# Performance work log

Measured on AMD Instinct MI355X. Metric: run time of the kernel, lower is better.

## Reference

```python
import jax, jax.numpy as jnp
import numpy as np

EPS = 1e-5

def layer_norm(x, g, b):
    mu = jnp.mean(x, axis=-1, keepdims=True)
    var = jnp.mean(jnp.square(x - mu), axis=-1, keepdims=True)
    return (x - mu) * jax.lax.rsqrt(var + EPS) * g + b

def setup_inputs() -> dict:
    key = jax.random.key(0)
    ks = jax.random.split(key, 8)
    B, T, D, H = 8, 2048, 32, 4
    hd = D // H
    s = 0.05
    return {
        "x": jax.random.normal(ks[0], (B, T, D), jnp.float32),
        "Wq": jax.random.normal(ks[1], (H, D, hd), jnp.float32) * s,
        "Wk": jax.random.normal(ks[2], (H, D, hd), jnp.float32) * s,
        "Wv": jax.random.normal(ks[3], (H, D, hd), jnp.float32) * s,
        "Wproj": jax.random.normal(ks[4], (D, D), jnp.float32) * s,
        "bproj": jnp.zeros((D,), jnp.float32),
        "ln1_g": jnp.ones((D,), jnp.float32),
        "ln1_b": jnp.zeros((D,), jnp.float32),
        "W1": jax.random.normal(ks[5], (D, 4 * D), jnp.float32) * s,
        "b1": jnp.zeros((4 * D,), jnp.float32),
        "W2": jax.random.normal(ks[6], (4 * D, D), jnp.float32) * s,
        "b2": jnp.zeros((D,), jnp.float32),
        "ln2_g": jnp.ones((D,), jnp.float32),
        "ln2_b": jnp.zeros((D,), jnp.float32),
    }

def reference(x, Wq, Wk, Wv, Wproj, bproj, ln1_g, ln1_b, W1, b1, W2, b2, ln2_g, ln2_b):
    B, T, D = x.shape
    H, _, hd = Wq.shape
    scale = hd ** -0.5
    # NOTE: original block normalizes first, and the residual uses the NORMALIZED x
    h = layer_norm(x, ln1_g, ln1_b)                      # (B,T,D)
    q = jnp.einsum('btd,hdk->bhtk', h, Wq)
    k = jnp.einsum('btd,hdk->bhtk', h, Wk)
    v = jnp.einsum('btd,hdk->bhtk', h, Wv)
    scores = jnp.einsum('bhtk,bhsk->bhts', q, k) * scale  # (B,H,T,T)
    mask = jnp.tril(jnp.ones((T, T), bool))
    scores = jnp.where(mask, scores, -jnp.inf)
    attn = jax.nn.softmax(scores, axis=-1)               # dropout = identity (eval)
    o = jnp.einsum('bhts,bhsk->bhtk', attn, v)           # (B,H,T,hd)
    o = o.transpose(0, 2, 1, 3).reshape(B, T, D)         # concat heads, head0 first
    x1 = h + o @ Wproj + bproj
    h2 = layer_norm(x1, ln2_g, ln2_b)
    ff = jax.nn.relu(h2 @ W1 + b1) @ W2 + b2             # dropout = identity (eval)
    return h2 + ff
```

## Files before the change

### kernel.cpp

```cpp
#include <hip/hip_runtime.h>
#include <math.h>

#define BB 8
#define TT 2048
#define DD 32
#define HH 4
#define HD 8
#define NROWS (BB*TT)
#define LNEPS 1e-5f

#if __has_builtin(__builtin_amdgcn_exp2f)
#define EXP2F(x) __builtin_amdgcn_exp2f(x)
#else
#define EXP2F(x) __expf(0.6931471805599453f*(x))
#endif

typedef _Float16 h2 __attribute__((ext_vector_type(2)));
typedef _Float16 h4v __attribute__((ext_vector_type(4)));
typedef _Float16 h8v __attribute__((ext_vector_type(8)));
typedef float f32x16 __attribute__((ext_vector_type(16)));
struct KH { h2 a, b, c, d; };
union F4H { float4 f; KH k; };

static __device__ __forceinline__ h2 pkrtz(float a, float b) {
    return __builtin_bit_cast(h2, __builtin_amdgcn_cvt_pkrtz(a, b));
}
static __device__ __forceinline__ unsigned pkrtz_u(float a, float b) {
    return __builtin_bit_cast(unsigned, __builtin_amdgcn_cvt_pkrtz(a, b));
}
static __device__ __forceinline__ unsigned short f16u(float x) {
    return __builtin_bit_cast(unsigned short, (_Float16)x);
}

#if __has_builtin(__builtin_amdgcn_fdot2)
#define DOT2(a,b,c) __builtin_amdgcn_fdot2((a),(b),(c),false)
#else
#define DOT2(a,b,c) fmaf((float)(a)[1],(float)(b)[1], fmaf((float)(a)[0],(float)(b)[0],(c)))
#endif

__global__ __launch_bounds__(256) void k_ln_qkv(
    const float* __restrict__ x,
    const float* __restrict__ Wq, const float* __restrict__ Wk, const float* __restrict__ Wv,
    const float* __restrict__ g, const float* __restrict__ b,
    float* __restrict__ h, float* __restrict__ qh,
    float* __restrict__ Kh, float* __restrict__ Vt)
{
    __shared__ float sW[3*HH*264];
    __shared__ float sg[DD], sb[DD];
    for (int i = threadIdx.x; i < HH*DD*HD; i += 256) {
        int hd_ = i >> 8, off = i & 255;
        sW[hd_*264 + off]              = Wq[i];
        sW[(4+hd_)*264 + off]          = Wk[i];
        sW[(8+hd_)*264 + off]          = Wv[i];
    }
    if (threadIdx.x < DD) { sg[threadIdx.x] = g[threadIdx.x]; sb[threadIdx.x] = b[threadIdx.x]; }
    __syncthreads();

    int idx = blockIdx.x * 256 + threadIdx.x;
    int r   = idx >> 3;
    int sub = idx & 7;
    int hh  = sub & 3;
    int dh  = sub >> 2;
    int bb  = r >> 11, tt = r & 2047;

    float xr[16];
    {
        const float4* xp = (const float4*)(x + (size_t)r * DD + dh*16);
        float4 t0 = xp[0], t1 = xp[1], t2 = xp[2], t3 = xp[3];
        xr[0]=t0.x; xr[1]=t0.y; xr[2]=t0.z; xr[3]=t0.w;
        xr[4]=t1.x; xr[5]=t1.y; xr[6]=t1.z; xr[7]=t1.w;
        xr[8]=t2.x; xr[9]=t2.y; xr[10]=t2.z; xr[11]=t2.w;
        xr[12]=t3.x; xr[13]=t3.y; xr[14]=t3.z; xr[15]=t3.w;
    }
    float s1 = 0.f;
    #pragma unroll
    for (int i = 0; i < 16; ++i) s1 += xr[i];
    s1 += __shfl_xor(s1, 4, 64);
    float mu = s1 * (1.f/DD);
    float sq = 0.f;
    #pragma unroll
    for (int i = 0; i < 16; ++i) { float d = xr[i]-mu; sq += d*d; }
    sq += __shfl_xor(sq, 4, 64);
    float rs = rsqrtf(sq * (1.f/DD) + LNEPS);

    float hr[16];
    #pragma unroll
    for (int i = 0; i < 16; ++i) hr[i] = (xr[i]-mu)*rs*sg[dh*16+i] + sb[dh*16+i];

    {
        float4* hp = (float4*)(h + (size_t)r * DD + dh*16);
        hp[0]=make_float4(hr[0],hr[1],hr[2],hr[3]);
        hp[1]=make_float4(hr[4],hr[5],hr[6],hr[7]);
        hp[2]=make_float4(hr[8],hr[9],hr[10],hr[11]);
        hp[3]=make_float4(hr[12],hr[13],hr[14],hr[15]);
    }

    const float* wq = sW + hh*264 + dh*128;
    const float* wk = sW + (4+hh)*264 + dh*128;
    const float* wv = sW + (8+hh)*264 + dh*128;
    float qa[HD], ka[HD], va[HD];
    #pragma unroll
    for (int k2 = 0; k2 < HD; ++k2) { qa[k2]=0.f; ka[k2]=0.f; va[k2]=0.f; }
    #pragma unroll
    for (int d = 0; d < 16; ++d) {
        float hv = hr[d];
        const float4* wq4 = (const float4*)(wq + d*8);
        const float4* wk4 = (const float4*)(wk + d*8);
        const float4* wv4 = (const float4*)(wv + d*8);
        float4 a0 = wq4[0], a1 = wq4[1];
        float4 b0 = wk4[0], b1 = wk4[1];
        float4 c0 = wv4[0], c1 = wv4[1];
        qa[0]=fmaf(hv,a0.x,qa[0]); qa[1]=fmaf(hv,a0.y,qa[1]); qa[2]=fmaf(hv,a0.z,qa[2]); qa[3]=fmaf(hv,a0.w,qa[3]);
        qa[4]=fmaf(hv,a1.x,qa[4]); qa[5]=fmaf(hv,a1.y,qa[5]); qa[6]=fmaf(hv,a1.z,qa[6]); qa[7]=fmaf(hv,a1.w,qa[7]);
        ka[0]=fmaf(hv,b0.x,ka[0]); ka[1]=fmaf(hv,b0.y,ka[1]); ka[2]=fmaf(hv,b0.z,ka[2]); ka[3]=fmaf(hv,b0.w,ka[3]);
        ka[4]=fmaf(hv,b1.x,ka[4]); ka[5]=fmaf(hv,b1.y,ka[5]); ka[6]=fmaf(hv,b1.z,ka[6]); ka[7]=fmaf(hv,b1.w,ka[7]);
        va[0]=fmaf(hv,c0.x,va[0]); va[1]=fmaf(hv,c0.y,va[1]); va[2]=fmaf(hv,c0.z,va[2]); va[3]=fmaf(hv,c0.w,va[3]);
        va[4]=fmaf(hv,c1.x,va[4]); va[5]=fmaf(hv,c1.y,va[5]); va[6]=fmaf(hv,c1.z,va[6]); va[7]=fmaf(hv,c1.w,va[7]);
    }
    #pragma unroll
    for (int k2 = 0; k2 < HD; ++k2) {
        qa[k2] += __shfl_xor(qa[k2], 4, 64);
        ka[k2] += __shfl_xor(ka[k2], 4, 64);
        va[k2] += __shfl_xor(va[k2], 4, 64);
    }

    const float SCL = 0.35355339059327373f * 1.4426950408889634f;
    size_t key = (size_t)(bb*HH + hh)*TT + tt;
    unsigned short* vtb = (unsigned short*)Vt + (size_t)(bb*HH + hh)*8*TT + tt;
    if (dh == 0) {
        F4H u;
        u.k.a = pkrtz(qa[0]*SCL, qa[1]*SCL);
        u.k.b = pkrtz(qa[2]*SCL, qa[3]*SCL);
        u.k.c = pkrtz(qa[4]*SCL, qa[5]*SCL);
        u.k.d = pkrtz(qa[6]*SCL, qa[7]*SCL);
        *(float4*)(qh + key*4) = u.f;
        vtb[(size_t)0*TT] = f16u(va[0]);
        vtb[(size_t)1*TT] = f16u(va[1]);
        vtb[(size_t)2*TT] = f16u(va[2]);
        vtb[(size_t)3*TT] = f16u(va[3]);
    } else {
        char* Kb8 = (char*)Kh + (size_t)(bb*HH + hh)*32768;
        uint2 k01; k01.x = pkrtz_u(ka[0],ka[1]); k01.y = pkrtz_u(ka[2],ka[3]);
        uint2 k23; k23.x = pkrtz_u(ka[4],ka[5]); k23.y = pkrtz_u(ka[6],ka[7]);
        *(uint2*)(Kb8 + (size_t)tt*8) = k01;
        *(uint2*)(Kb8 + 16384 + (size_t)tt*8) = k23;
        vtb[(size_t)4*TT] = f16u(va[4]);
        vtb[(size_t)5*TT] = f16u(va[5]);
        vtb[(size_t)6*TT] = f16u(va[6]);
        vtb[(size_t)7*TT] = f16u(va[7]);
    }
}

template<bool DIAG>
__device__ __forceinline__ void chunk_compute(
    uint2 kraw, uint4 v0r, uint4 v1r, int hi, int col,
    h4v qf, float& m, float& l, f32x16& acc)
{
    h4v kf = __builtin_bit_cast(h4v, kraw);
    f32x16 cin;
    #pragma unroll
    for (int r2 = 0; r2 < 16; ++r2) cin[r2] = -m;
    f32x16 S = __builtin_amdgcn_mfma_f32_32x32x8f16(kf, qf, cin, 0, 0, 0);
    if (DIAG) {
        #pragma unroll
        for (int r2 = 0; r2 < 16; ++r2) {
            int row = (r2&3) + 8*(r2>>2) + 4*hi;
            if (row > col) S[r2] = -1e30f;
        }
    }
    float pm = S[0];
    #pragma unroll
    for (int r2 = 1; r2 < 16; ++r2) pm = fmaxf(pm, S[r2]);
    pm = fmaxf(pm, __shfl_xor(pm, 32, 64));
    if (__builtin_expect(__any(pm > 8.f), 0)) {
        float adj = fmaxf(pm, 0.f);
        float cr  = EXP2F(-adj);
        l *= cr;
        #pragma unroll
        for (int r2 = 0; r2 < 16; ++r2) {
            int row = (r2&3) + 8*(r2>>2) + 4*hi;
            acc[r2] *= __shfl(cr, row, 64);
        }
        #pragma unroll
        for (int r2 = 0; r2 < 16; ++r2) S[r2] -= adj;
        m += adj;
    }
    float p[16];
    #pragma unroll
    for (int r2 = 0; r2 < 16; ++r2) p[r2] = EXP2F(S[r2]);
    unsigned pa_ = pkrtz_u(p[0],  p[1]);
    unsigned pb_ = pkrtz_u(p[2],  p[3]);
    unsigned pc_ = pkrtz_u(p[4],  p[5]);
    unsigned pd_ = pkrtz_u(p[6],  p[7]);
    unsigned pe_ = pkrtz_u(p[8],  p[9]);
    unsigned pf_ = pkrtz_u(p[10], p[11]);
    unsigned pg_ = pkrtz_u(p[12], p[13]);
    unsigned ph_ = pkrtz_u(p[14], p[15]);
    const h2 one2 = {(_Float16)1.f, (_Float16)1.f};
    l = DOT2(__builtin_bit_cast(h2, pa_), one2, l);
    l = DOT2(__builtin_bit_cast(h2, pb_), one2, l);
    l = DOT2(__builtin_bit_cast(h2, pc_), one2, l);
    l = DOT2(__builtin_bit_cast(h2, pd_), one2, l);
    l = DOT2(__builtin_bit_cast(h2, pe_), one2, l);
    l = DOT2(__builtin_bit_cast(h2, pf_), one2, l);
    l = DOT2(__builtin_bit_cast(h2, pg_), one2, l);
    l = DOT2(__builtin_bit_cast(h2, ph_), one2, l);
    unsigned ra = (unsigned)__shfl_xor((int)pa_, 32, 64);
    unsigned rb = (unsigned)__shfl_xor((int)pb_, 32, 64);
    unsigned rc = (unsigned)__shfl_xor((int)pc_, 32, 64);
    unsigned rd = (unsigned)__shfl_xor((int)pd_, 32, 64);
    unsigned re = (unsigned)__shfl_xor((int)pe_, 32, 64);
    unsigned rf = (unsigned)__shfl_xor((int)pf_, 32, 64);
    unsigned rg = (unsigned)__shfl_xor((int)pg_, 32, 64);
    unsigned rh = (unsigned)__shfl_xor((int)ph_, 32, 64);
    bool H = (hi != 0);
    uint4 A0 = { H?rc:pa_, H?rd:pb_, H?pc_:ra, H?pd_:rb };
    uint4 A1 = { H?rg:pe_, H?rh:pf_, H?pg_:re, H?ph_:rf };
    acc = __builtin_amdgcn_mfma_f32_32x32x16_f16(
        __builtin_bit_cast(h8v, A0), __builtin_bit_cast(h8v, v0r), acc, 0, 0, 0);
    acc = __builtin_amdgcn_mfma_f32_32x32x16_f16(
        __builtin_bit_cast(h8v, A1), __builtin_bit_cast(h8v, v1r), acc, 0, 0, 0);
}

__global__ __launch_bounds__(256) void k_attn(
    const float* __restrict__ qh, const float* __restrict__ Kh,
    const float* __restrict__ Vt, float* __restrict__ o)
{
    __shared__ float mb[128];
    __shared__ float lb[128];
    __shared__ float ob[512];
    const int tid  = threadIdx.x;
    const int wave = tid >> 6;
    const int lane = tid & 63;
    const int hi   = lane >> 5;
    const int col  = lane & 31;
    const int tl   = wave >> 1;
    const int p    = wave & 1;
    const int T    = blockIdx.x * 2 + tl;
    const int qi   = 63 - (T >> 5);
    const int bh   = T & 31;
    const int wq0  = qi << 5;

    const char* Kg = (const char*)Kh + (size_t)bh * 32768;
    const char* Vg = (const char*)Vt + (size_t)bh * 32768;
    const char* Qg = (const char*)qh + (size_t)bh * 32768 + (size_t)wq0 * 16;
    const char* vrow = Vg + (size_t)(col & 7) * 4096;

    h4v qf = __builtin_bit_cast(h4v, *(const uint2*)(Qg + col*16 + hi*8));

    f32x16 acc;
    #pragma unroll
    for (int r2 = 0; r2 < 16; ++r2) acc[r2] = 0.f;
    float m = 0.f, l = 0.f;

#define LOADC(c, K2, V0, V1) do { \
    K2 = *(const uint2*)(Kg + hi*16384 + (size_t)((((c)<<5) + col))*8); \
    V0 = *(const uint4*)(vrow + (size_t)((((c)<<5) + (hi<<3)))*2); \
    V1 = *(const uint4*)(vrow + (size_t)((((c)<<5) + 16 + (hi<<3)))*2); \
} while (0)

    const int last = ((qi & 1) == p) ? qi : qi - 1;
    if (last >= p) {
        uint2 kc_; uint4 v0c, v1c;
        LOADC(p, kc_, v0c, v1c);
        int c = p;
        while (c < last) {
            uint2 kn_; uint4 v0n, v1n;
            LOADC(c + 2, kn_, v0n, v1n);
            chunk_compute<false>(kc_, v0c, v1c, hi, col, qf, m, l, acc);
            kc_ = kn_; v0c = v0n; v1c = v1n;
            c += 2;
        }
        if (last == qi) chunk_compute<true >(kc_, v0c, v1c, hi, col, qf, m, l, acc);
        else            chunk_compute<false>(kc_, v0c, v1c, hi, col, qf, m, l, acc);
    }
#undef LOADC

    l += __shfl_xor(l, 32, 64);
    if (lane < 32) {
        mb[tl*64 + p*32 + col] = m;
        lb[tl*64 + p*32 + col] = l;
    }
    __syncthreads();
    float mo = mb[tl*64 + (p^1)*32 + col];
    float lo = lb[tl*64 + (p^1)*32 + col];
    float M  = fmaxf(m, mo);
    float fs = EXP2F(m - M);
    float L  = l * fs + lo * EXP2F(mo - M);
    float Linv = 1.f / L;
    float fr[16], Lr[16];
    #pragma unroll
    for (int r2 = 0; r2 < 16; ++r2) {
        int row = (r2&3) + 8*(r2>>2) + 4*hi;
        fr[r2] = __shfl(fs,   row, 64);
        Lr[r2] = __shfl(Linv, row, 64);
    }
    if (p == 1 && col < HD) {
        #pragma unroll
        for (int r2 = 0; r2 < 16; ++r2) {
            int row = (r2&3) + 8*(r2>>2) + 4*hi;
            ob[tl*256 + (row<<3) + col] = acc[r2] * fr[r2];
        }
    }
    __syncthreads();
    if (p == 0 && col < HD) {
        float* og = o + ((size_t)bh*TT + wq0)*HD + col;
        #pragma unroll
        for (int r2 = 0; r2 < 16; ++r2) {
            int row = (r2&3) + 8*(r2>>2) + 4*hi;
            og[(size_t)row * HD] = (acc[r2]*fr[r2] + ob[tl*256 + (row<<3) + col]) * Lr[r2];
        }
    }
}

__global__ __launch_bounds__(256) void k_proj_ffn(
    const float* __restrict__ h, const float* __restrict__ o,
    const float* __restrict__ Wproj, const float* __restrict__ bproj,
    const float* __restrict__ W1, const float* __restrict__ b1,
    const float* __restrict__ W2, const float* __restrict__ b2,
    const float* __restrict__ g2, const float* __restrict__ bt2,
    float* __restrict__ out)
{
    __shared__ float sWp[DD*36], sW1T[4*DD*36], sW2[4*DD*36];
    __shared__ float sbp[DD], sb1[4*DD], sb2[DD], sg2[DD], sbt2[DD];
    for (int i = threadIdx.x; i < DD*DD; i += 256)      sWp [(i>>5)*36 + (i&31)] = Wproj[i];
    for (int i = threadIdx.x; i < DD*4*DD; i += 256) {
        sW1T[(i&127)*36 + (i>>7)] = W1[i];
        sW2 [(i>>5)*36 + (i&31)]  = W2[i];
    }
    if (threadIdx.x < DD) {
        sbp[threadIdx.x]  = bproj[threadIdx.x];
        sb2[threadIdx.x]  = b2[threadIdx.x];
        sg2[threadIdx.x]  = g2[threadIdx.x];
        sbt2[threadIdx.x] = bt2[threadIdx.x];
    }
    if (threadIdx.x < 4*DD) sb1[threadIdx.x] = b1[threadIdx.x];
    __syncthreads();

    int idx = blockIdx.x * 256 + threadIdx.x;
    int r   = idx >> 3;
    int sub = idx & 7;
    int bb  = r >> 11, tt = r & 2047;

    float o4[4];
    #pragma unroll
    for (int mm = 0; mm < 4; ++mm)
        o4[mm] = o[((size_t)(bb*HH + mm)*TT + tt) * HD + sub];

    float x1[DD];
    #pragma unroll
    for (int d = 0; d < DD; ++d) x1[d] = 0.f;
    #pragma unroll
    for (int mm = 0; mm < 4; ++mm) {
        const float4* wr = (const float4*)&sWp[(sub + 8*mm)*36];
        float ov = o4[mm];
        #pragma unroll
        for (int dc = 0; dc < 8; ++dc) {
            float4 w4 = wr[dc];
            x1[4*dc]   = fmaf(ov, w4.x, x1[4*dc]);
            x1[4*dc+1] = fmaf(ov, w4.y, x1[4*dc+1]);
            x1[4*dc+2] = fmaf(ov, w4.z, x1[4*dc+2]);
            x1[4*dc+3] = fmaf(ov, w4.w, x1[4*dc+3]);
        }
    }
    #pragma unroll
    for (int d = 0; d < DD; ++d) {
        x1[d] += __shfl_xor(x1[d], 1, 64);
        x1[d] += __shfl_xor(x1[d], 2, 64);
        x1[d] += __shfl_xor(x1[d], 4, 64);
    }
    {
        const float4* hp = (const float4*)(h + (size_t)r * DD);
        #pragma unroll
        for (int dc = 0; dc < 8; ++dc) {
            float4 h4 = hp[dc];
            x1[4*dc]   += h4.x + sbp[4*dc];
            x1[4*dc+1] += h4.y + sbp[4*dc+1];
            x1[4*dc+2] += h4.z + sbp[4*dc+2];
            x1[4*dc+3] += h4.w + sbp[4*dc+3];
        }
    }
    float mu = 0.f;
    #pragma unroll
    for (int d = 0; d < DD; ++d) mu += x1[d];
    mu *= (1.f/DD);
    float var = 0.f;
    #pragma unroll
    for (int d = 0; d < DD; ++d) { float dl = x1[d]-mu; var += dl*dl; }
    var *= (1.f/DD);
    float rs = rsqrtf(var + LNEPS);
    float h2v[DD];
    #pragma unroll
    for (int d = 0; d < DD; ++d) h2v[d] = (x1[d]-mu)*rs*sg2[d] + sbt2[d];

    float outp[DD];
    #pragma unroll
    for (int d = 0; d < DD; ++d) outp[d] = 0.f;
    #pragma unroll
    for (int mm = 0; mm < 16; ++mm) {
        int j = sub + 8*mm;
        const float4* w1r = (const float4*)&sW1T[j*36];
        float a = sb1[j];
        #pragma unroll
        for (int dc = 0; dc < 8; ++dc) {
            float4 w4 = w1r[dc];
            a = fmaf(h2v[4*dc], w4.x, a);
            a = fmaf(h2v[4*dc+1], w4.y, a);
            a = fmaf(h2v[4*dc+2], w4.z, a);
            a = fmaf(h2v[4*dc+3], w4.w, a);
        }
        a = fmaxf(a, 0.f);
        const float4* w2r = (const float4*)&sW2[j*36];
        #pragma unroll
        for (int dc = 0; dc < 8; ++dc) {
            float4 w4 = w2r[dc];
            outp[4*dc]   = fmaf(a, w4.x, outp[4*dc]);
            outp[4*dc+1] = fmaf(a, w4.y, outp[4*dc+1]);
            outp[4*dc+2] = fmaf(a, w4.z, outp[4*dc+2]);
            outp[4*dc+3] = fmaf(a, w4.w, outp[4*dc+3]);
        }
    }
    if (sub == 0) {
        #pragma unroll
        for (int d = 0; d < DD; ++d) outp[d] += h2v[d] + sb2[d];
    }
    float t1[16];
    #pragma unroll
    for (int i = 0; i < 16; ++i) {
        bool hib = (sub & 4) != 0;
        float send = hib ? outp[i] : outp[i+16];
        float recv = __shfl_xor(send, 4, 64);
        t1[i] = (hib ? outp[i+16] : outp[i]) + recv;
    }
    float t2[8];
    #pragma unroll
    for (int i = 0; i < 8; ++i) {
        bool hib = (sub & 2) != 0;
        float send = hib ? t1[i] : t1[i+8];
        float recv = __shfl_xor(send, 2, 64);
        t2[i] = (hib ? t1[i+8] : t1[i]) + recv;
    }
    float w0[4];
    #pragma unroll
    for (int i = 0; i < 4; ++i) {
        bool hib = (sub & 1) != 0;
        float send = hib ? t2[i] : t2[i+4];
        float recv = __shfl_xor(send, 1, 64);
        w0[i] = (hib ? t2[i+4] : t2[i]) + recv;
    }
    *(float4*)(out + (size_t)r * DD + sub*4) = make_float4(w0[0], w0[1], w0[2], w0[3]);
}

extern "C" void kernel_launch(void* const* d_in, const int* in_sizes, int n_in,
                              void* d_out, int out_size, void* d_ws, size_t ws_size,
                              hipStream_t stream) {
    const float* x     = (const float*)d_in[0];
    const float* Wq    = (const float*)d_in[1];
    const float* Wk    = (const float*)d_in[2];
    const float* Wv    = (const float*)d_in[3];
    const float* Wproj = (const float*)d_in[4];
    const float* bproj = (const float*)d_in[5];
    const float* ln1_g = (const float*)d_in[6];
    const float* ln1_b = (const float*)d_in[7];
    const float* W1    = (const float*)d_in[8];
    const float* b1    = (const float*)d_in[9];
    const float* W2    = (const float*)d_in[10];
    const float* b2    = (const float*)d_in[11];
    const float* ln2_g = (const float*)d_in[12];
    const float* ln2_b = (const float*)d_in[13];
    float* out = (float*)d_out;

    const size_t N = (size_t)NROWS * DD;
    const size_t K = (size_t)BB*HH*TT*4;
    float* ws = (float*)d_ws;
    float* h  = ws;
    float* qh = ws + N;
    float* Kh = ws + N + K;
    float* Vt = ws + N + 2*K;
    float* o  = ws + N + 3*K;

    k_ln_qkv  <<<512, 256, 0, stream>>>(x, Wq, Wk, Wv, ln1_g, ln1_b, h, qh, Kh, Vt);
    k_attn    <<<1024, 256, 0, stream>>>(qh, Kh, Vt, o);
    k_proj_ffn<<<512, 256, 0, stream>>>(h, o, Wproj, bproj, W1, b1, W2, b2, ln2_g, ln2_b, out);
}
```

Measured before the change: 123.0 us.

## Split each attention query tile's KV chunks across four waves instead of two

Each block now handles one 32-query tile, and its four waves each take every fourth KV chunk. Before, a block held two tiles with two waves per tile. The partial max, sum and output of the four waves are merged through shared memory with a four-way softmax combine. This doubles the grid and shortens the serial chunk loop per wave, which targets latency on the longer causal rows. The cost is more merge work, extra shared-memory traffic, and waves on short tiles that have little or no work.

```diff
diff --git a/kernel.cpp b/kernel.cpp
--- a/kernel.cpp
+++ b/kernel.cpp
@@ -226,17 +226,15 @@
     const float* __restrict__ qh, const float* __restrict__ Kh,
     const float* __restrict__ Vt, float* __restrict__ o)
 {
-    __shared__ float mb[128];
-    __shared__ float lb[128];
-    __shared__ float ob[512];
+    __shared__ float mb[4][32];
+    __shared__ float lb[4][32];
+    __shared__ float ob[3][256];
     const int tid  = threadIdx.x;
-    const int wave = tid >> 6;
+    const int p    = tid >> 6;
     const int lane = tid & 63;
     const int hi   = lane >> 5;
     const int col  = lane & 31;
-    const int tl   = wave >> 1;
-    const int p    = wave & 1;
-    const int T    = blockIdx.x * 2 + tl;
+    const int T    = blockIdx.x;
     const int qi   = 63 - (T >> 5);
     const int bh   = T & 31;
     const int wq0  = qi << 5;
@@ -259,17 +257,17 @@
     V1 = *(const uint4*)(vrow + (size_t)((((c)<<5) + 16 + (hi<<3)))*2); \
 } while (0)
 
-    const int last = ((qi & 1) == p) ? qi : qi - 1;
-    if (last >= p) {
+    if (qi >= p) {
+        const int last = qi - ((qi - p) & 3);
         uint2 kc_; uint4 v0c, v1c;
         LOADC(p, kc_, v0c, v1c);
         int c = p;
         while (c < last) {
             uint2 kn_; uint4 v0n, v1n;
-            LOADC(c + 2, kn_, v0n, v1n);
+            LOADC(c + 4, kn_, v0n, v1n);
             chunk_compute<false>(kc_, v0c, v1c, hi, col, qf, m, l, acc);
             kc_ = kn_; v0c = v0n; v1c = v1n;
-            c += 2;
+            c += 4;
         }
         if (last == qi) chunk_compute<true >(kc_, v0c, v1c, hi, col, qf, m, l, acc);
         else            chunk_compute<false>(kc_, v0c, v1c, hi, col, qf, m, l, acc);
@@ -277,16 +275,13 @@
 #undef LOADC
 
     l += __shfl_xor(l, 32, 64);
-    if (lane < 32) {
-        mb[tl*64 + p*32 + col] = m;
-        lb[tl*64 + p*32 + col] = l;
-    }
+    if (lane < 32) { mb[p][col] = m; lb[p][col] = l; }
     __syncthreads();
-    float mo = mb[tl*64 + (p^1)*32 + col];
-    float lo = lb[tl*64 + (p^1)*32 + col];
-    float M  = fmaxf(m, mo);
+    float m0 = mb[0][col], m1 = mb[1][col], m2 = mb[2][col], m3 = mb[3][col];
+    float M  = fmaxf(fmaxf(m0, m1), fmaxf(m2, m3));
+    float L  = lb[0][col]*EXP2F(m0-M) + lb[1][col]*EXP2F(m1-M)
+             + lb[2][col]*EXP2F(m2-M) + lb[3][col]*EXP2F(m3-M);
     float fs = EXP2F(m - M);
-    float L  = l * fs + lo * EXP2F(mo - M);
     float Linv = 1.f / L;
     float fr[16], Lr[16];
     #pragma unroll
@@ -295,11 +290,11 @@
         fr[r2] = __shfl(fs,   row, 64);
         Lr[r2] = __shfl(Linv, row, 64);
     }
-    if (p == 1 && col < HD) {
+    if (p > 0 && col < HD) {
         #pragma unroll
         for (int r2 = 0; r2 < 16; ++r2) {
             int row = (r2&3) + 8*(r2>>2) + 4*hi;
-            ob[tl*256 + (row<<3) + col] = acc[r2] * fr[r2];
+            ob[p-1][(row<<3) + col] = acc[r2] * fr[r2];
         }
     }
     __syncthreads();
@@ -308,7 +303,9 @@
         #pragma unroll
         for (int r2 = 0; r2 < 16; ++r2) {
             int row = (r2&3) + 8*(r2>>2) + 4*hi;
-            og[(size_t)row * HD] = (acc[r2]*fr[r2] + ob[tl*256 + (row<<3) + col]) * Lr[r2];
+            int ix = (row<<3) + col;
+            og[(size_t)row * HD] =
+                (acc[r2]*fr[r2] + ob[0][ix] + ob[1][ix] + ob[2][ix]) * Lr[r2];
         }
     }
 }
@@ -480,6 +477,6 @@
     float* o  = ws + N + 3*K;
 
     k_ln_qkv  <<<512, 256, 0, stream>>>(x, Wq, Wk, Wv, ln1_g, ln1_b, h, qh, Kh, Vt);
-    k_attn    <<<1024, 256, 0, stream>>>(qh, Kh, Vt, o);
+    k_attn    <<<2048, 256, 0, stream>>>(qh, Kh, Vt, o);
     k_proj_ffn<<<512, 256, 0, stream>>>(h, o, Wproj, bproj, W1, b1, W2, b2, ln2_g, ln2_b, out);
 }
```

Result: slower. 126.8 us (+3.1%).
